# Kernel optimization log

Measured on AMD Instinct MI355X. Metric: run time of the kernel, lower is better.

## Reference

```python
import jax, jax.numpy as jnp
import numpy as np
from jax import lax

DN = ('NCHW', 'OIHW', 'NCHW')
CORRKS = 7
CORR_DIL = 4

def _conv(x, w, pad, dil=1):
    return lax.conv_general_dilated(x, w, (1, 1), [(pad, pad), (pad, pad)],
                                    rhs_dilation=(dil, dil), dimension_numbers=DN)

def _lrelu(x):
    return jnp.where(x >= 0, x, 0.1 * x)

def _bn(x):
    # BatchNorm2d(affine=False), training-mode batch statistics, eps=1e-5
    m = x.mean((0, 2, 3), keepdims=True)
    v = ((x - m) ** 2).mean((0, 2, 3), keepdims=True)
    return (x - m) * lax.rsqrt(v + 1e-5)

def _gauss1d():
    # kornia gaussian(13, sigma=3): exp(-x^2/(2*sigma^2)), normalized
    x = jnp.arange(13, dtype=jnp.float32) - 6.0
    g = jnp.exp(-(x * x) / 18.0)
    return g / g.sum()

def _blur13(x, mode):
    # separable 13x13 gaussian (sigma=3) depthwise; mode: 'constant' or 'edge'
    c = x.shape[1]
    g = _gauss1d()
    xp = jnp.pad(x, ((0, 0), (0, 0), (6, 6), (6, 6)), mode=mode)
    kh = jnp.broadcast_to(g.reshape(1, 1, 13, 1), (c, 1, 13, 1))
    kw = jnp.broadcast_to(g.reshape(1, 1, 1, 13), (c, 1, 1, 13))
    y = lax.conv_general_dilated(xp, kh, (1, 1), 'VALID', dimension_numbers=DN,
                                 feature_group_count=c)
    y = lax.conv_general_dilated(y, kw, (1, 1), 'VALID', dimension_numbers=DN,
                                 feature_group_count=c)
    return y

def _localcorr(f1, f2, w_fc1, w_fc2):
    b, c, h, w = f2.shape
    feat = _lrelu(_conv(jnp.concatenate([f1, f2], axis=1), w_fc1, 1))
    feat = _conv(feat, w_fc2, 1)
    f1s = _blur13(f1, 'constant')
    # F.unfold(kernel=7, dilation=4, padding=12): gather 49 shifted views
    pad = 2 * (CORRKS - 1)  # 12
    f1p = jnp.pad(f1s, ((0, 0), (0, 0), (pad, pad), (pad, pad)), mode='constant')
    lc = []
    for di in range(CORRKS):
        for dj in range(CORRKS):
            sh = lax.dynamic_slice(f1p, (0, 0, di * CORR_DIL, dj * CORR_DIL), (b, c, h, w))
            lc.append(((f2 - sh) ** 2).mean(axis=1))  # (b,h,w)
    lc = jnp.stack(lc, axis=1)  # (b,49,h,w), kernel-position order = ki*7+kj
    return jnp.concatenate([feat, lc], axis=1)  # (b, c+49, h, w)

def _forward(feat1, feat2, w_pre, w_fc1, w_fc2, w_e0, w_e1, w_e2, w_e3):
    b, c, h, w = feat1.shape
    feat = _conv(jnp.concatenate([feat1, feat2], axis=0), w_pre, 1, 1)
    f1, f2 = feat[:b], feat[b:]
    corr = _localcorr(f1, f2, w_fc1, w_fc2)
    corr = _lrelu(_bn(_conv(corr, w_e0, 1, 1)))
    corr = _lrelu(_bn(_conv(corr, w_e1, 2, 2)))
    corr = _lrelu(_bn(_conv(corr, w_e2, 4, 4)))
    corr = _conv(corr, w_e3, 1, 1)
    corr = _blur13(corr, 'edge')
    disp = jnp.clip(corr, -300.0, 300.0)
    scale = jnp.array([w - 1, h - 1], dtype=jnp.float32).reshape(1, 2, 1, 1)
    return disp / scale

def setup_inputs() -> dict:
    key = jax.random.key(0)
    ks = jax.random.split(key, 9)
    B, C, H, W = 4, 64, 256, 256
    def wconv(k, oc, ic):
        std = (ic * 9) ** -0.5
        return jax.random.normal(k, (oc, ic, 3, 3), dtype=jnp.float32) * std
    return {
        'feat1': jax.random.normal(ks[0], (B, C, H, W), dtype=jnp.float32),
        'feat2': jax.random.normal(ks[1], (B, C, H, W), dtype=jnp.float32),
        'w_pre': wconv(ks[2], C, C),
        'w_fc1': wconv(ks[3], 2 * C, 2 * C),
        'w_fc2': wconv(ks[4], C, 2 * C),
        'w_e0': wconv(ks[5], 32, C + 49),
        'w_e1': wconv(ks[6], 16, 32),
        'w_e2': wconv(ks[7], 8, 16),
        'w_e3': wconv(ks[8], 2, 8),
    }

def reference(feat1, feat2, w_pre, w_fc1, w_fc2, w_e0, w_e1, w_e2, w_e3):
    return _forward(feat1, feat2, w_pre, w_fc1, w_fc2, w_e0, w_e1, w_e2, w_e3)
```

## Files before the change

kernel.cpp:

```cpp
#include <hip/hip_runtime.h>
#include <hip/hip_cooperative_groups.h>
#include <math.h>

namespace cg = cooperative_groups;

#define HWS 16

typedef __attribute__((address_space(1))) const float gas_float;
typedef __attribute__((address_space(3))) float las_float;

__device__ __forceinline__ void gload_lds16(const float* src, float* ldsb) {
  __builtin_amdgcn_global_load_lds((gas_float*)src, (las_float*)ldsb, 16, 0, 0);
}

__device__ __forceinline__ float wsum(float v) {
#pragma unroll
  for (int o = 32; o > 0; o >>= 1) v += __shfl_down(v, o, 64);
  return v;
}

__device__ void fill_gauss(float* g) {
  if (threadIdx.x < 13) {
    double ssum = 0.0;
    for (int i = 0; i < 13; ++i) { double xi = (double)i - 6.0; ssum += exp(-(xi * xi) / 18.0); }
    double xk = (double)threadIdx.x - 6.0;
    g[threadIdx.x] = (float)(exp(-(xk * xk) / 18.0) / ssum);
  }
  __syncthreads();
}

template<int OCB, int ICB, int DIL>
__device__ void conv_stage(const float* __restrict__ in0, int ic0,
                           const float* __restrict__ in1,
                           const float* __restrict__ wt,
                           float* __restrict__ out,
                           int nS, int IC, int OC, int act,
                           float* s, const float* zp)
{
  constexpr int IWP = 40;
  constexpr int IH = 8 + 2 * DIL;
  constexpr int CHP = IWP * IH;
  constexpr int UPC = CHP / 4;
  const int tid = threadIdx.x;
  const int tx = tid & 31, ty = tid >> 5;
  const int zc = OC / OCB;
  const int ic1n = IC - ic0;
  const int nTiles = 8 * 32 * nS * zc;

  for (int t = blockIdx.x; t < nTiles; t += gridDim.x) {
    const int bx = t & 7, r1 = t >> 3;
    const int by = r1 & 31, z = r1 >> 5;
    const int n = z / zc, ocBase = (z % zc) * OCB;
    const int x0 = bx * 32, y0 = by * 8;

    float acc[OCB];
#pragma unroll
    for (int j = 0; j < OCB; ++j) acc[j] = 0.f;

    for (int icg = 0; icg < IC; icg += ICB) {
      const int gcnt = (IC - icg < ICB) ? (IC - icg) : ICB;
      const int units = gcnt * UPC;
      const int nrounds = (units + 255) >> 8;
      for (int k = 0; k < nrounds; ++k) {
        if ((k << 8) + (tid & 192) < units) {
          const int j = (k << 8) + tid;
          const int jj = (j < units) ? j : 0;
          const int ch = jj / UPC, r2 = jj - ch * UPC;
          const int row = r2 / 10, cb = r2 - row * 10;
          const int ic = icg + ch;
          const float* inc = (ic < ic0)
              ? in0 + ((size_t)(n * ic0 + ic) << HWS)
              : in1 + ((size_t)(n * ic1n + (ic - ic0)) << HWS);
          const int gy = y0 - DIL + row;
          const int gx0 = x0 - 4 + (cb << 2);
          const bool ok = (j < units) && gy >= 0 && gy < 256 && gx0 >= 0 && gx0 < 256;
          const float* src = ok ? (inc + gy * 256 + gx0) : zp;
          gload_lds16(src, s + (k << 10) + ((tid & 192) << 2));
        }
      }
      __syncthreads();
      for (int u = 0; u < gcnt; ++u) {
        float xi[9];
#pragma unroll
        for (int ky = 0; ky < 3; ++ky)
#pragma unroll
          for (int kx = 0; kx < 3; ++kx)
            xi[ky * 3 + kx] = s[u * CHP + (ty + ky * DIL) * IWP + tx + 4 + (kx - 1) * DIL];
        const float* wp = wt + ((size_t)ocBase * IC + (icg + u)) * 9;
#pragma unroll
        for (int j = 0; j < OCB; ++j) {
          const float* wj = wp + (size_t)j * IC * 9;
          float a = acc[j];
#pragma unroll
          for (int q = 0; q < 9; ++q) a = fmaf(xi[q], wj[q], a);
          acc[j] = a;
        }
      }
      __syncthreads();
    }
    const size_t pix = (size_t)(y0 + ty) * 256 + x0 + tx;
#pragma unroll
    for (int j = 0; j < OCB; ++j) {
      float v = acc[j];
      if (act) v = (v >= 0.f) ? v : 0.1f * v;
      out[((size_t)(n * OC + ocBase + j) << HWS) + pix] = v;
    }
  }
}

__device__ void lc_stage(const float* __restrict__ f1s, const float* __restrict__ f2,
                         float* __restrict__ lc, float* s, const float* zp)
{
  const int tid = threadIdx.x;
  const int tx = tid & 31, ty = tid >> 5;
  for (int t = blockIdx.x; t < 256; t += gridDim.x) {
    const int x0 = (t & 7) * 32, y0 = (t >> 3) * 8;
    const size_t pix = (size_t)(y0 + ty) * 256 + x0 + tx;
    float acc[49];
#pragma unroll
    for (int d = 0; d < 49; ++d) acc[d] = 0.f;
    for (int c = 0; c < 64; ++c) {
      const float* b1 = f1s + ((size_t)c << HWS);
      float f2v = f2[((size_t)c << HWS) + pix];
#pragma unroll
      for (int k = 0; k < 2; ++k) {
        if ((k << 8) + (tid & 192) < 448) {
          const int j = (k << 8) + tid;
          const int row = j / 14, cb = j - row * 14;
          const int gy = y0 - 12 + row;
          const int gx0 = x0 - 12 + (cb << 2);
          const bool ok = gy >= 0 && gy < 256 && gx0 >= 0 && gx0 < 256;
          const float* src = ok ? (b1 + gy * 256 + gx0) : zp;
          gload_lds16(src, s + (k << 10) + ((tid & 192) << 2));
        }
      }
      __syncthreads();
#pragma unroll
      for (int di = 0; di < 7; ++di)
#pragma unroll
        for (int dj = 0; dj < 7; ++dj) {
          float v = s[(ty + di * 4) * 56 + tx + dj * 4];
          float df = f2v - v;
          acc[di * 7 + dj] = fmaf(df, df, acc[di * 7 + dj]);
        }
      __syncthreads();
    }
#pragma unroll
    for (int d = 0; d < 49; ++d)
      lc[((size_t)d << HWS) + pix] = acc[d] * (1.f / 64.f);
  }
}

__device__ void blur_fused_stage(const float* __restrict__ in, float* __restrict__ out,
                                 const float* g, int nPlanes, int mode, int fin, float* s)
{
  const int tid = threadIdx.x;
  const int tx = tid & 31, ty = tid >> 5;
  const int nT = nPlanes << 8;
  for (int t = blockIdx.x; t < nT; t += gridDim.x) {
    const int tile = t & 255, pl = t >> 8;
    const int x0 = (tile & 7) * 32, y0 = (tile >> 3) * 8;
    const float* base = in + ((size_t)pl << HWS);
    for (int i = tid; i < 880; i += 256) {
      int rr = i / 44, cc = i - rr * 44;
      int gy = y0 - 6 + rr, gx = x0 - 6 + cc;
      float v = 0.f;
      if (mode) {
        gy = gy < 0 ? 0 : (gy > 255 ? 255 : gy);
        gx = gx < 0 ? 0 : (gx > 255 ? 255 : gx);
        v = base[gy * 256 + gx];
      } else if (gy >= 0 && gy < 256 && gx >= 0 && gx < 256) {
        v = base[gy * 256 + gx];
      }
      s[i] = v;
    }
    __syncthreads();
    for (int i = tid; i < 352; i += 256) {
      int r = i / 44, c = i - r * 44;
      float a = 0.f;
#pragma unroll
      for (int k = 0; k < 13; ++k) a = fmaf(g[k], s[(r + k) * 44 + c], a);
      s[880 + i] = a;
    }
    __syncthreads();
    {
      float a = 0.f;
#pragma unroll
      for (int k = 0; k < 13; ++k) a = fmaf(g[k], s[880 + ty * 44 + tx + k], a);
      if (fin) a = fminf(fmaxf(a, -300.f), 300.f) * (1.0f / 255.0f);
      out[((size_t)pl << HWS) + (size_t)(y0 + ty) * 256 + x0 + tx] = a;
    }
    __syncthreads();
  }
}

__device__ void bn_partial_stage(const float* __restrict__ x, float2* part, int C, float* sm)
{
  for (int job = blockIdx.x; job < C * 64; job += gridDim.x) {
    const int c = job >> 6, pb = job & 63;
    const int e0 = pb * 4096;
    float s = 0.f, q = 0.f;
    for (int i = threadIdx.x; i < 4096; i += 256) {
      int e = e0 + i;
      int nn = e >> HWS, p = e & 65535;
      float v = x[((size_t)(nn * C + c) << HWS) + p];
      s += v;
      q = fmaf(v, v, q);
    }
    s = wsum(s); q = wsum(q);
    __syncthreads();
    if ((threadIdx.x & 63) == 0) { sm[threadIdx.x >> 6] = s; sm[4 + (threadIdx.x >> 6)] = q; }
    __syncthreads();
    if (threadIdx.x == 0)
      part[job] = make_float2(sm[0] + sm[1] + sm[2] + sm[3], sm[4] + sm[5] + sm[6] + sm[7]);
  }
}

__device__ void bn_apply_stage(float* x, const float2* __restrict__ part, int C, float* sst)
{
  for (int c = threadIdx.x; c < C; c += 256) {
    float s = 0.f, q = 0.f;
    for (int p = 0; p < 64; ++p) { float2 pp = part[c * 64 + p]; s += pp.x; q += pp.y; }
    const float inv = 1.0f / (4.0f * 65536.0f);
    float m = s * inv;
    float var = q * inv - m * m;
    sst[2 * c] = m;
    sst[2 * c + 1] = 1.0f / sqrtf(var + 1e-5f);
  }
  __syncthreads();
  const int total = (4 * C) << HWS;
  for (int idx = blockIdx.x * 256 + threadIdx.x; idx < total; idx += gridDim.x * 256) {
    int c = (idx >> HWS) % C;
    float v = (x[idx] - sst[2 * c]) * sst[2 * c + 1];
    x[idx] = v >= 0.f ? v : 0.1f * v;
  }
  __syncthreads();
}

__global__ void __launch_bounds__(256, 8) disp_mega(
    const float* __restrict__ feat1, const float* __restrict__ feat2,
    const float* __restrict__ w_pre, const float* __restrict__ w_fc1,
    const float* __restrict__ w_fc2, const float* __restrict__ w_e0,
    const float* __restrict__ w_e1, const float* __restrict__ w_e2,
    const float* __restrict__ w_e3,
    float* __restrict__ outp,
    float* A, float* B, float* L, float* T, float* U,
    float2* part, float* zp)
{
  cg::grid_group grid = cg::this_grid();
  __shared__ float smem[4096];
  __shared__ float gtab[13];
  __shared__ float bnsm[8];
  __shared__ float sst[64];

  float* e0b = B;
  float* e1b = B + 8388608;
  float* e2b = B + 12582912;
  float* e3b = B + 14680064;

  if (threadIdx.x < 64) zp[threadIdx.x] = 0.f;
  fill_gauss(gtab);

  conv_stage<16, 10, 1>(feat1, 64, nullptr, w_pre, A, 4, 64, 64, 0, smem, zp);
  conv_stage<16, 10, 1>(feat2, 64, nullptr, w_pre, B, 4, 64, 64, 0, smem, zp);
  grid.sync();

  for (int n = 0; n < 4; ++n) {
    const float* f1n = A + ((size_t)(n * 64) << HWS);
    float* f1nw = A + ((size_t)(n * 64) << HWS);
    const float* f2n = B + ((size_t)(n * 64) << HWS);
    float* lcn = L + ((size_t)(n * 49) << HWS);

    conv_stage<16, 10, 1>(f1n, 64, f2n, w_fc1, T, 1, 128, 128, 1, smem, zp);
    blur_fused_stage(f1n, U, gtab, 64, 0, 0, smem);
    grid.sync();

    lc_stage(U, f2n, lcn, smem, zp);
    conv_stage<16, 10, 1>(T, 128, nullptr, w_fc2, f1nw, 1, 128, 64, 0, smem, zp);
    grid.sync();
  }

  conv_stage<16, 10, 1>(A, 64, L, w_e0, e0b, 4, 113, 32, 0, smem, zp);
  grid.sync();
  bn_partial_stage(e0b, part, 32, bnsm);
  grid.sync();
  bn_apply_stage(e0b, part, 32, sst);
  grid.sync();

  conv_stage<16, 8, 2>(e0b, 32, nullptr, w_e1, e1b, 4, 32, 16, 0, smem, zp);
  grid.sync();
  bn_partial_stage(e1b, part, 16, bnsm);
  grid.sync();
  bn_apply_stage(e1b, part, 16, sst);
  grid.sync();

  conv_stage<8, 4, 4>(e1b, 16, nullptr, w_e2, e2b, 4, 16, 8, 0, smem, zp);
  grid.sync();
  bn_partial_stage(e2b, part, 8, bnsm);
  grid.sync();
  bn_apply_stage(e2b, part, 8, sst);
  grid.sync();

  conv_stage<2, 10, 1>(e2b, 8, nullptr, w_e3, e3b, 4, 8, 2, 0, smem, zp);
  grid.sync();

  blur_fused_stage(e3b, outp, gtab, 8, 1, 1, smem);
}

extern "C" void kernel_launch(void* const* d_in, const int* in_sizes, int n_in,
                              void* d_out, int out_size, void* d_ws, size_t ws_size,
                              hipStream_t stream)
{
  const float* feat1 = (const float*)d_in[0];
  const float* feat2 = (const float*)d_in[1];
  const float* w_pre = (const float*)d_in[2];
  const float* w_fc1 = (const float*)d_in[3];
  const float* w_fc2 = (const float*)d_in[4];
  const float* w_e0  = (const float*)d_in[5];
  const float* w_e1  = (const float*)d_in[6];
  const float* w_e2  = (const float*)d_in[7];
  const float* w_e3  = (const float*)d_in[8];
  float* outp = (float*)d_out;

  const size_t offA = 0;
  const size_t offB = 67108864;
  const size_t offL = 134217728;
  const size_t offT = 185597952;
  const size_t offU = 219152384;
  const size_t offP = 235929856;
  const size_t offZ = 235946496;
  const size_t needed = 235946752;
  if (ws_size < needed) return;

  char* ws = (char*)d_ws;
  float* A = (float*)(ws + offA);
  float* B = (float*)(ws + offB);
  float* L = (float*)(ws + offL);
  float* T = (float*)(ws + offT);
  float* U = (float*)(ws + offU);
  float2* part = (float2*)(ws + offP);
  float* zp = (float*)(ws + offZ);

  int nb = 0;
  hipOccupancyMaxActiveBlocksPerMultiprocessor(&nb, (const void*)disp_mega, 256, 0);
  if (nb < 1) nb = 1;
  long long g = (long long)nb * 256;
  if (g > 4096) g = 4096;

  void* args[] = { (void*)&feat1, (void*)&feat2, (void*)&w_pre, (void*)&w_fc1,
                   (void*)&w_fc2, (void*)&w_e0, (void*)&w_e1, (void*)&w_e2,
                   (void*)&w_e3, (void*)&outp, (void*)&A, (void*)&B, (void*)&L,
                   (void*)&T, (void*)&U, (void*)&part, (void*)&zp };
  hipLaunchCooperativeKernel((const void*)disp_mega, dim3((unsigned)g), dim3(256),
                             args, 0, stream);
}
```

Measured before the change: 6.961 ms.

## Double-buffer LDS staging in conv and local-correlation stages

Splits the shared-memory staging buffer into two halves, so the async global-to-LDS loads for the next channel group are issued while the current group is being computed. This removes one barrier per iteration. The input-channel group sizes are halved so that each buffer still fits in the 4096-float shared array. In exchange, each group needs more iterations, so per-group overhead and weight-load granularity rise, and a barrier is added at the end of each tile.

After: 23.62 ms. 3.39x slower.

```diff
diff --git a/kernel.cpp b/kernel.cpp
--- a/kernel.cpp
+++ b/kernel.cpp
@@ -41,11 +41,13 @@
   constexpr int IH = 8 + 2 * DIL;
   constexpr int CHP = IWP * IH;
   constexpr int UPC = CHP / 4;
+  constexpr int SBUF = 2048;
   const int tid = threadIdx.x;
   const int tx = tid & 31, ty = tid >> 5;
   const int zc = OC / OCB;
   const int ic1n = IC - ic0;
   const int nTiles = 8 * 32 * nS * zc;
+  const int ngrp = (IC + ICB - 1) / ICB;
 
   for (int t = blockIdx.x; t < nTiles; t += gridDim.x) {
     const int bx = t & 7, r1 = t >> 3;
@@ -57,10 +59,11 @@
 #pragma unroll
     for (int j = 0; j < OCB; ++j) acc[j] = 0.f;
 
-    for (int icg = 0; icg < IC; icg += ICB) {
-      const int gcnt = (IC - icg < ICB) ? (IC - icg) : ICB;
-      const int units = gcnt * UPC;
+    auto stage = [&](int icg, int bufsel) {
+      const int gcnt2 = (IC - icg < ICB) ? (IC - icg) : ICB;
+      const int units = gcnt2 * UPC;
       const int nrounds = (units + 255) >> 8;
+      float* sb = s + bufsel * SBUF;
       for (int k = 0; k < nrounds; ++k) {
         if ((k << 8) + (tid & 192) < units) {
           const int j = (k << 8) + tid;
@@ -75,18 +78,25 @@
           const int gx0 = x0 - 4 + (cb << 2);
           const bool ok = (j < units) && gy >= 0 && gy < 256 && gx0 >= 0 && gx0 < 256;
           const float* src = ok ? (inc + gy * 256 + gx0) : zp;
-          gload_lds16(src, s + (k << 10) + ((tid & 192) << 2));
+          gload_lds16(src, sb + (k << 10) + ((tid & 192) << 2));
         }
       }
+    };
+
+    stage(0, 0);
+    for (int g = 0; g < ngrp; ++g) {
       __syncthreads();
+      if (g + 1 < ngrp) stage(g * ICB + ICB, (g + 1) & 1);
+      const float* sb = s + (g & 1) * SBUF;
+      const int gcnt = (IC - g * ICB < ICB) ? (IC - g * ICB) : ICB;
       for (int u = 0; u < gcnt; ++u) {
         float xi[9];
 #pragma unroll
         for (int ky = 0; ky < 3; ++ky)
 #pragma unroll
           for (int kx = 0; kx < 3; ++kx)
-            xi[ky * 3 + kx] = s[u * CHP + (ty + ky * DIL) * IWP + tx + 4 + (kx - 1) * DIL];
-        const float* wp = wt + ((size_t)ocBase * IC + (icg + u)) * 9;
+            xi[ky * 3 + kx] = sb[u * CHP + (ty + ky * DIL) * IWP + tx + 4 + (kx - 1) * DIL];
+        const float* wp = wt + ((size_t)ocBase * IC + (g * ICB + u)) * 9;
 #pragma unroll
         for (int j = 0; j < OCB; ++j) {
           const float* wj = wp + (size_t)j * IC * 9;
@@ -96,7 +106,6 @@
           acc[j] = a;
         }
       }
-      __syncthreads();
     }
     const size_t pix = (size_t)(y0 + ty) * 256 + x0 + tx;
 #pragma unroll
@@ -105,12 +114,14 @@
       if (act) v = (v >= 0.f) ? v : 0.1f * v;
       out[((size_t)(n * OC + ocBase + j) << HWS) + pix] = v;
     }
+    __syncthreads();
   }
 }
 
 __device__ void lc_stage(const float* __restrict__ f1s, const float* __restrict__ f2,
                          float* __restrict__ lc, float* s, const float* zp)
 {
+  constexpr int SBUF = 2048;
   const int tid = threadIdx.x;
   const int tx = tid & 31, ty = tid >> 5;
   for (int t = blockIdx.x; t < 256; t += gridDim.x) {
@@ -119,9 +130,10 @@
     float acc[49];
 #pragma unroll
     for (int d = 0; d < 49; ++d) acc[d] = 0.f;
-    for (int c = 0; c < 64; ++c) {
+
+    auto stage = [&](int c, int bufsel) {
       const float* b1 = f1s + ((size_t)c << HWS);
-      float f2v = f2[((size_t)c << HWS) + pix];
+      float* sb = s + bufsel * SBUF;
 #pragma unroll
       for (int k = 0; k < 2; ++k) {
         if ((k << 8) + (tid & 192) < 448) {
@@ -131,23 +143,30 @@
           const int gx0 = x0 - 12 + (cb << 2);
           const bool ok = gy >= 0 && gy < 256 && gx0 >= 0 && gx0 < 256;
           const float* src = ok ? (b1 + gy * 256 + gx0) : zp;
-          gload_lds16(src, s + (k << 10) + ((tid & 192) << 2));
+          gload_lds16(src, sb + (k << 10) + ((tid & 192) << 2));
         }
       }
+    };
+
+    stage(0, 0);
+    for (int c = 0; c < 64; ++c) {
+      float f2v = f2[((size_t)c << HWS) + pix];
       __syncthreads();
+      if (c + 1 < 64) stage(c + 1, (c + 1) & 1);
+      const float* sb = s + (c & 1) * SBUF;
 #pragma unroll
       for (int di = 0; di < 7; ++di)
 #pragma unroll
         for (int dj = 0; dj < 7; ++dj) {
-          float v = s[(ty + di * 4) * 56 + tx + dj * 4];
+          float v = sb[(ty + di * 4) * 56 + tx + dj * 4];
           float df = f2v - v;
           acc[di * 7 + dj] = fmaf(df, df, acc[di * 7 + dj]);
         }
-      __syncthreads();
     }
 #pragma unroll
     for (int d = 0; d < 49; ++d)
       lc[((size_t)d << HWS) + pix] = acc[d] * (1.f / 64.f);
+    __syncthreads();
   }
 }
 
@@ -261,8 +280,8 @@
   if (threadIdx.x < 64) zp[threadIdx.x] = 0.f;
   fill_gauss(gtab);
 
-  conv_stage<16, 10, 1>(feat1, 64, nullptr, w_pre, A, 4, 64, 64, 0, smem, zp);
-  conv_stage<16, 10, 1>(feat2, 64, nullptr, w_pre, B, 4, 64, 64, 0, smem, zp);
+  conv_stage<16, 5, 1>(feat1, 64, nullptr, w_pre, A, 4, 64, 64, 0, smem, zp);
+  conv_stage<16, 5, 1>(feat2, 64, nullptr, w_pre, B, 4, 64, 64, 0, smem, zp);
   grid.sync();
 
   for (int n = 0; n < 4; ++n) {
@@ -271,37 +290,37 @@
     const float* f2n = B + ((size_t)(n * 64) << HWS);
     float* lcn = L + ((size_t)(n * 49) << HWS);
 
-    conv_stage<16, 10, 1>(f1n, 64, f2n, w_fc1, T, 1, 128, 128, 1, smem, zp);
+    conv_stage<16, 5, 1>(f1n, 64, f2n, w_fc1, T, 1, 128, 128, 1, smem, zp);
     blur_fused_stage(f1n, U, gtab, 64, 0, 0, smem);
     grid.sync();
 
     lc_stage(U, f2n, lcn, smem, zp);
-    conv_stage<16, 10, 1>(T, 128, nullptr, w_fc2, f1nw, 1, 128, 64, 0, smem, zp);
+    conv_stage<16, 5, 1>(T, 128, nullptr, w_fc2, f1nw, 1, 128, 64, 0, smem, zp);
     grid.sync();
   }
 
-  conv_stage<16, 10, 1>(A, 64, L, w_e0, e0b, 4, 113, 32, 0, smem, zp);
+  conv_stage<16, 5, 1>(A, 64, L, w_e0, e0b, 4, 113, 32, 0, smem, zp);
   grid.sync();
   bn_partial_stage(e0b, part, 32, bnsm);
   grid.sync();
   bn_apply_stage(e0b, part, 32, sst);
   grid.sync();
 
-  conv_stage<16, 8, 2>(e0b, 32, nullptr, w_e1, e1b, 4, 32, 16, 0, smem, zp);
+  conv_stage<16, 4, 2>(e0b, 32, nullptr, w_e1, e1b, 4, 32, 16, 0, smem, zp);
   grid.sync();
   bn_partial_stage(e1b, part, 16, bnsm);
   grid.sync();
   bn_apply_stage(e1b, part, 16, sst);
   grid.sync();
 
-  conv_stage<8, 4, 4>(e1b, 16, nullptr, w_e2, e2b, 4, 16, 8, 0, smem, zp);
+  conv_stage<8, 3, 4>(e1b, 16, nullptr, w_e2, e2b, 4, 16, 8, 0, smem, zp);
   grid.sync();
   bn_partial_stage(e2b, part, 8, bnsm);
   grid.sync();
   bn_apply_stage(e2b, part, 8, sst);
   grid.sync();
 
-  conv_stage<2, 10, 1>(e2b, 8, nullptr, w_e3, e3b, 4, 8, 2, 0, smem, zp);
+  conv_stage<2, 5, 1>(e2b, 8, nullptr, w_e3, e3b, 4, 8, 2, 0, smem, zp);
   grid.sync();
 
   blur_fused_stage(e3b, outp, gtab, 8, 1, 1, smem);
```
